# Kernel optimization log

Hardware: AMD Instinct MI355X
Metric: run time of the kernel (lower is better)

The kernel has to match this reference:

```python
import jax, jax.numpy as jnp
import numpy as np

B, IN, HID, OUT = 1024, 256, 512, 2
MU_INIT, LOGVAR_INIT = 0.0, -5.0
VAR_MIN = 1e-6


def setup_inputs() -> dict:
    key = jax.random.key(0)
    ks = jax.random.split(key, 9)
    inp = {
        "x": jax.random.normal(ks[0], (B, IN), dtype=jnp.float32),
        "w1_mu": MU_INIT + 0.1 * jax.random.normal(ks[1], (HID, IN), dtype=jnp.float32),
        "w1_logvar": LOGVAR_INIT + 0.1 * jax.random.normal(ks[2], (HID, IN), dtype=jnp.float32),
        "b1_mu": MU_INIT + 0.1 * jax.random.normal(ks[3], (HID,), dtype=jnp.float32),
        "b1_logvar": LOGVAR_INIT + 0.1 * jax.random.normal(ks[4], (HID,), dtype=jnp.float32),
        "w2_mu": MU_INIT + 0.1 * jax.random.normal(ks[5], (OUT, HID), dtype=jnp.float32),
        "w2_logvar": LOGVAR_INIT + 0.1 * jax.random.normal(ks[6], (OUT, HID), dtype=jnp.float32),
        "b2_mu": MU_INIT + 0.1 * jax.random.normal(ks[7], (OUT,), dtype=jnp.float32),
        "b2_logvar": LOGVAR_INIT + 0.1 * jax.random.normal(ks[8], (OUT,), dtype=jnp.float32),
    }
    return inp


def _bayes_linear(x, w_mu, w_logvar, b_mu, b_logvar, eps_w, eps_b):
    # Non-efficient path: per-example sampled weights (batch, out, in) and biases (batch, out)
    w_std = jnp.exp(0.5 * w_logvar)
    b_std = jnp.exp(0.5 * b_logvar)
    weights = w_mu[None, :, :] + w_std[None, :, :] * eps_w  # (B, O, I)
    biases = b_mu[None, :] + b_std[None, :] * eps_b          # (B, O)
    out = jnp.einsum("boi,bi->bo", weights, x)
    return out + biases


def reference(x, w1_mu, w1_logvar, b1_mu, b1_logvar, w2_mu, w2_logvar, b2_mu, b2_logvar):
    # Noise sampled inside forward, matching torch.randn in the module (fixed key for determinism)
    nk = jax.random.split(jax.random.key(42), 4)
    eps_w1 = jax.random.normal(nk[0], (B, HID, IN), dtype=x.dtype)
    eps_b1 = jax.random.normal(nk[1], (B, HID), dtype=x.dtype)
    eps_w2 = jax.random.normal(nk[2], (B, OUT, HID), dtype=x.dtype)
    eps_b2 = jax.random.normal(nk[3], (B, OUT), dtype=x.dtype)

    h = jax.nn.relu(_bayes_linear(x, w1_mu, w1_logvar, b1_mu, b1_logvar, eps_w1, eps_b1))
    out = _bayes_linear(h, w2_mu, w2_logvar, b2_mu, b2_logvar, eps_w2, eps_b2)  # (B, 2)
    mean = out[:, 0]
    var = jnp.maximum(jnp.exp(out[:, 1]), VAR_MIN)
    return mean, var
```

## Files before the change

kernel.cpp:

```cpp
#include <hip/hip_runtime.h>
#include <stdint.h>

#define BATCH 1024
#define IN    256
#define HID   512
#define OUT   2

#define SQRT2 1.4142135623730951

__host__ __device__ __forceinline__ uint32_t rotl32(uint32_t x, uint32_t r) {
#ifdef __HIP_DEVICE_COMPILE__
    return __builtin_rotateleft32(x, r);
#else
    return (x << r) | (x >> (32 - r));
#endif
}

__host__ __device__ __forceinline__ void threefry2x32(uint32_t k0, uint32_t k1,
                                                      uint32_t& x0, uint32_t& x1) {
    uint32_t k2 = k0 ^ k1 ^ 0x1BD11BDAu;
    x0 += k0; x1 += k1;
#define TF_R(r) { x0 += x1; x1 = rotl32(x1, (r)); x1 ^= x0; }
    TF_R(13) TF_R(15) TF_R(26) TF_R(6)   x0 += k1; x1 += k2 + 1u;
    TF_R(17) TF_R(29) TF_R(16) TF_R(24)  x0 += k2; x1 += k0 + 2u;
    TF_R(13) TF_R(15) TF_R(26) TF_R(6)   x0 += k0; x1 += k1 + 3u;
    TF_R(17) TF_R(29) TF_R(16) TF_R(24)  x0 += k1; x1 += k2 + 4u;
    TF_R(13) TF_R(15) TF_R(26) TF_R(6)   x0 += k2; x1 += k0 + 5u;
#undef TF_R
}

struct TFK {
    uint32_t k0, k1, k2, i1b, i2b, i3b, i4b, i5b;
    uint32_t k1j0, k1j1, k1j2, k1j3;
    uint32_t K01j0, K01j1, K01j2, K01j3;
    __device__ __forceinline__ TFK(uint32_t a, uint32_t b) {
        k0 = a; k1 = b; k2 = a ^ b ^ 0x1BD11BDAu;
        i1b = k2 + 1u; i2b = k0 + 2u; i3b = k1 + 3u; i4b = k2 + 4u; i5b = k0 + 5u;
        k1j0 = k1;        k1j1 = k1 + 1u;   k1j2 = k1 + 2u;   k1j3 = k1 + 3u;
        uint32_t K01 = k0 + k1;
        K01j0 = K01;      K01j1 = K01 + 1u; K01j2 = K01 + 2u; K01j3 = K01 + 3u;
    }
};

__device__ __forceinline__ uint32_t tf_core(const TFK& K, uint32_t cnt,
                                            uint32_t k1j, uint32_t K01j) {
    uint32_t t  = cnt + k1j;
    uint32_t x0 = cnt + K01j;
    uint32_t x1 = rotl32(t, 13) ^ x0;
    x0 += x1; x1 = rotl32(x1, 15) ^ x0;
    x0 += x1; x1 = rotl32(x1, 26) ^ x0;
    x0 += x1; x1 = rotl32(x1,  6) ^ x0;
    t = x1 + K.i1b; x0 = x0 + t + K.k1;  x1 = rotl32(t, 17) ^ x0;
    x0 += x1; x1 = rotl32(x1, 29) ^ x0;
    x0 += x1; x1 = rotl32(x1, 16) ^ x0;
    x0 += x1; x1 = rotl32(x1, 24) ^ x0;
    t = x1 + K.i2b; x0 = x0 + t + K.k2;  x1 = rotl32(t, 13) ^ x0;
    x0 += x1; x1 = rotl32(x1, 15) ^ x0;
    x0 += x1; x1 = rotl32(x1, 26) ^ x0;
    x0 += x1; x1 = rotl32(x1,  6) ^ x0;
    t = x1 + K.i3b; x0 = x0 + t + K.k0;  x1 = rotl32(t, 17) ^ x0;
    x0 += x1; x1 = rotl32(x1, 29) ^ x0;
    x0 += x1; x1 = rotl32(x1, 16) ^ x0;
    x0 += x1; x1 = rotl32(x1, 24) ^ x0;
    t = x1 + K.i4b; x0 = x0 + t + K.k1;  x1 = rotl32(t, 13) ^ x0;
    x0 += x1; x1 = rotl32(x1, 15) ^ x0;
    x0 += x1; x1 = rotl32(x1, 26) ^ x0;
    x0 += x1; x1 = rotl32(x1,  6) ^ x0;
    return (x0 + K.k2) ^ (x1 + K.i5b);
}
__device__ __forceinline__ uint32_t tf_bits(const TFK& K, uint32_t cnt) {
    return tf_core(K, cnt, K.k1j0, K.K01j0);
}

__device__ __forceinline__ float bits_to_normal(uint32_t bits) {
    const float LO = -0.99999994f;
#if __has_builtin(__builtin_amdgcn_alignbit)
    float m = __uint_as_float(__builtin_amdgcn_alignbit(0x7Fu, bits, 9u));
#else
    float m = __uint_as_float((bits >> 9) | 0x3f800000u);
#endif
    float u = fmaxf(LO, fmaf(m, 2.0f, -3.0f));
    float z = fmaf(-u, u, 1.0f);
    float L = __log2f(z);
    float wa = fmaf(L, -0.69314718f, -2.5f);
    float p = (float)(0.00021858087 * SQRT2);
    p = fmaf(p, wa, (float)(-0.00125372503 * SQRT2));
    p = fmaf(p, wa, (float)(-0.00417768164 * SQRT2));
    p = fmaf(p, wa, (float)(0.246640727 * SQRT2));
    p = fmaf(p, wa, (float)(1.50140941 * SQRT2));
    return p * u;
}

__global__ __launch_bounds__(256) void k_w1std(const float* __restrict__ w1_logvar,
                                               float* __restrict__ w1_std) {
    int i = blockIdx.x * 256 + threadIdx.x;
    if (i < HID * IN) w1_std[i] = __expf(0.5f * w1_logvar[i]);
}

__global__ __launch_bounds__(256, 4) void k_layer1(
    const float* __restrict__ x, const float* __restrict__ w1_mu,
    const float* __restrict__ w1_std, const float* __restrict__ b1_mu,
    const float* __restrict__ b1_logvar, float* __restrict__ h,
    uint32_t kw0, uint32_t kw1, uint32_t kb0, uint32_t kb1)
{
    __shared__ float xs[IN];
    const int b = blockIdx.y;
    const int o = blockIdx.x * 256 + threadIdx.x;
    xs[threadIdx.x] = x[b * IN + threadIdx.x];
    __syncthreads();

    const TFK Kw(kw0, kw1);
    const float4* wm4 = (const float4*)(w1_mu  + o * IN);
    const float4* ws4 = (const float4*)(w1_std + o * IN);
    const float4* x4  = (const float4*)xs;

    uint32_t c = (uint32_t)(b * HID + o) * IN;
    float acc = 0.f;

    float4 m4 = wm4[0], s4 = ws4[0], xv = x4[0];
    #pragma unroll 3
    for (int i4 = 0; i4 < IN / 4 - 1; ++i4) {
        float4 m4n = wm4[i4 + 1], s4n = ws4[i4 + 1], xvn = x4[i4 + 1];
        float e0 = bits_to_normal(tf_core(Kw, c, Kw.k1j0, Kw.K01j0));
        float e1 = bits_to_normal(tf_core(Kw, c, Kw.k1j1, Kw.K01j1));
        float e2 = bits_to_normal(tf_core(Kw, c, Kw.k1j2, Kw.K01j2));
        float e3 = bits_to_normal(tf_core(Kw, c, Kw.k1j3, Kw.K01j3));
        c += 4u;
        acc = fmaf(fmaf(s4.x, e0, m4.x), xv.x, acc);
        acc = fmaf(fmaf(s4.y, e1, m4.y), xv.y, acc);
        acc = fmaf(fmaf(s4.z, e2, m4.z), xv.z, acc);
        acc = fmaf(fmaf(s4.w, e3, m4.w), xv.w, acc);
        m4 = m4n; s4 = s4n; xv = xvn;
    }
    {
        float e0 = bits_to_normal(tf_core(Kw, c, Kw.k1j0, Kw.K01j0));
        float e1 = bits_to_normal(tf_core(Kw, c, Kw.k1j1, Kw.K01j1));
        float e2 = bits_to_normal(tf_core(Kw, c, Kw.k1j2, Kw.K01j2));
        float e3 = bits_to_normal(tf_core(Kw, c, Kw.k1j3, Kw.K01j3));
        acc = fmaf(fmaf(s4.x, e0, m4.x), xv.x, acc);
        acc = fmaf(fmaf(s4.y, e1, m4.y), xv.y, acc);
        acc = fmaf(fmaf(s4.z, e2, m4.z), xv.z, acc);
        acc = fmaf(fmaf(s4.w, e3, m4.w), xv.w, acc);
    }
    const TFK Kb(kb0, kb1);
    float eb = bits_to_normal(tf_bits(Kb, (uint32_t)(b * HID + o)));
    float hv = acc + fmaf(__expf(0.5f * b1_logvar[o]), eb, b1_mu[o]);
    h[b * HID + o] = fmaxf(hv, 0.f);
}

__global__ __launch_bounds__(256) void k_layer2(
    const float* __restrict__ h, const float* __restrict__ w2_mu,
    const float* __restrict__ w2_logvar, const float* __restrict__ b2_mu,
    const float* __restrict__ b2_logvar, float* __restrict__ out,
    uint32_t kw0, uint32_t kw1, uint32_t kb0, uint32_t kb1)
{
    const int wave = (blockIdx.x * 256 + threadIdx.x) >> 6;
    const int lane = threadIdx.x & 63;
    const int b = wave >> 1, j = wave & 1;
    const TFK Kw(kw0, kw1);

    float acc = 0.f;
    #pragma unroll
    for (int oi = 0; oi < HID / 64; ++oi) {
        int o = oi * 64 + lane;
        uint32_t c = (uint32_t)((b * OUT + j) * HID + o);
        float e = bits_to_normal(tf_bits(Kw, c));
        float m = w2_mu[j * HID + o];
        float s = __expf(0.5f * w2_logvar[j * HID + o]);
        acc = fmaf(fmaf(s, e, m), h[b * HID + o], acc);
    }
    #pragma unroll
    for (int off = 32; off > 0; off >>= 1)
        acc += __shfl_down(acc, off, 64);
    if (lane == 0) {
        const TFK Kb(kb0, kb1);
        float eb = bits_to_normal(tf_bits(Kb, (uint32_t)(b * OUT + j)));
        float o0 = acc + fmaf(__expf(0.5f * b2_logvar[j]), eb, b2_mu[j]);
        if (j == 0) out[b] = o0;
        else        out[1024 + b] = fmaxf(__expf(o0), 1e-6f);
    }
}

extern "C" void kernel_launch(void* const* d_in, const int* in_sizes, int n_in,
                              void* d_out, int out_size, void* d_ws, size_t ws_size,
                              hipStream_t stream) {
    (void)in_sizes; (void)n_in; (void)out_size; (void)ws_size;
    const float* x         = (const float*)d_in[0];
    const float* w1_mu     = (const float*)d_in[1];
    const float* w1_logvar = (const float*)d_in[2];
    const float* b1_mu     = (const float*)d_in[3];
    const float* b1_logvar = (const float*)d_in[4];
    const float* w2_mu     = (const float*)d_in[5];
    const float* w2_logvar = (const float*)d_in[6];
    const float* b2_mu     = (const float*)d_in[7];
    const float* b2_logvar = (const float*)d_in[8];
    float* out = (float*)d_out;

    float* ws_w1std = (float*)d_ws;
    float* ws_h     = (float*)d_ws + HID * IN;

    uint32_t nk[4][2];
    for (uint32_t i = 0; i < 4; ++i) {
        uint32_t a = 0u, c = i;
        threefry2x32(0u, 42u, a, c);
        nk[i][0] = a; nk[i][1] = c;
    }
    const uint32_t kw1a = nk[0][0], kw1b = nk[0][1];
    const uint32_t kb1a = nk[1][0], kb1b = nk[1][1];
    const uint32_t kw2a = nk[2][0], kw2b = nk[2][1];
    const uint32_t kb2a = nk[3][0], kb2b = nk[3][1];

    k_w1std<<<(HID * IN + 255) / 256, 256, 0, stream>>>(w1_logvar, ws_w1std);
    k_layer1<<<dim3(2, 1024), 256, 0, stream>>>(x, w1_mu, ws_w1std, b1_mu, b1_logvar,
                                                ws_h, kw1a, kw1b, kb1a, kb1b);
    k_layer2<<<512, 256, 0, stream>>>(ws_h, w2_mu, w2_logvar, b2_mu, b2_logvar,
                                      out, kw2a, kw2b, kb2a, kb2b);
}
```

Measured before the change: 316.8 us.

## Fuse layer-2 dot product into layer-1 kernel with partial sums and epilogue

Layer 1 now computes each hidden activation and immediately multiplies it by the sampled layer-2 weights. Each block reduces its two partial outputs through wave shuffles and shared memory and writes them to a small partials buffer. A tiny epilogue kernel adds the two block partials, applies the sampled output bias and writes mean and variance. This removes the hidden-activation write/read and replaces the heavier layer-2 kernel, at the cost of an extra sync and more register use in layer 1.

```diff
diff --git a/kernel.cpp b/kernel.cpp
--- a/kernel.cpp
+++ b/kernel.cpp
@@ -100,10 +100,14 @@
 __global__ __launch_bounds__(256, 4) void k_layer1(
     const float* __restrict__ x, const float* __restrict__ w1_mu,
     const float* __restrict__ w1_std, const float* __restrict__ b1_mu,
-    const float* __restrict__ b1_logvar, float* __restrict__ h,
-    uint32_t kw0, uint32_t kw1, uint32_t kb0, uint32_t kb1)
+    const float* __restrict__ b1_logvar,
+    const float* __restrict__ w2_mu, const float* __restrict__ w2_logvar,
+    float* __restrict__ partials,
+    uint32_t kw0, uint32_t kw1, uint32_t kb0, uint32_t kb1,
+    uint32_t k2w0, uint32_t k2w1)
 {
     __shared__ float xs[IN];
+    __shared__ float red[8];
     const int b = blockIdx.y;
     const int o = blockIdx.x * 256 + threadIdx.x;
     xs[threadIdx.x] = x[b * IN + threadIdx.x];
@@ -144,41 +148,44 @@
     }
     const TFK Kb(kb0, kb1);
     float eb = bits_to_normal(tf_bits(Kb, (uint32_t)(b * HID + o)));
-    float hv = acc + fmaf(__expf(0.5f * b1_logvar[o]), eb, b1_mu[o]);
-    h[b * HID + o] = fmaxf(hv, 0.f);
-}
-
-__global__ __launch_bounds__(256) void k_layer2(
-    const float* __restrict__ h, const float* __restrict__ w2_mu,
-    const float* __restrict__ w2_logvar, const float* __restrict__ b2_mu,
+    float hv = fmaxf(acc + fmaf(__expf(0.5f * b1_logvar[o]), eb, b1_mu[o]), 0.f);
+
+    const TFK K2(k2w0, k2w1);
+    uint32_t c2 = (uint32_t)(b * OUT) * HID + (uint32_t)o;
+    float e20 = bits_to_normal(tf_bits(K2, c2));
+    float e21 = bits_to_normal(tf_bits(K2, c2 + HID));
+    float a0 = fmaf(__expf(0.5f * w2_logvar[o]),       e20, w2_mu[o])       * hv;
+    float a1 = fmaf(__expf(0.5f * w2_logvar[HID + o]), e21, w2_mu[HID + o]) * hv;
+
+    #pragma unroll
+    for (int off = 32; off > 0; off >>= 1) {
+        a0 += __shfl_down(a0, off, 64);
+        a1 += __shfl_down(a1, off, 64);
+    }
+    const int wv = threadIdx.x >> 6, ln = threadIdx.x & 63;
+    if (ln == 0) { red[wv] = a0; red[4 + wv] = a1; }
+    __syncthreads();
+    if (threadIdx.x == 0) {
+        float* p = partials + ((size_t)blockIdx.x * BATCH + b) * 2;
+        p[0] = (red[0] + red[1]) + (red[2] + red[3]);
+        p[1] = (red[4] + red[5]) + (red[6] + red[7]);
+    }
+}
+
+__global__ __launch_bounds__(256) void k_epilogue(
+    const float* __restrict__ partials, const float* __restrict__ b2_mu,
     const float* __restrict__ b2_logvar, float* __restrict__ out,
-    uint32_t kw0, uint32_t kw1, uint32_t kb0, uint32_t kb1)
+    uint32_t kb0, uint32_t kb1)
 {
-    const int wave = (blockIdx.x * 256 + threadIdx.x) >> 6;
-    const int lane = threadIdx.x & 63;
-    const int b = wave >> 1, j = wave & 1;
-    const TFK Kw(kw0, kw1);
-
-    float acc = 0.f;
-    #pragma unroll
-    for (int oi = 0; oi < HID / 64; ++oi) {
-        int o = oi * 64 + lane;
-        uint32_t c = (uint32_t)((b * OUT + j) * HID + o);
-        float e = bits_to_normal(tf_bits(Kw, c));
-        float m = w2_mu[j * HID + o];
-        float s = __expf(0.5f * w2_logvar[j * HID + o]);
-        acc = fmaf(fmaf(s, e, m), h[b * HID + o], acc);
-    }
-    #pragma unroll
-    for (int off = 32; off > 0; off >>= 1)
-        acc += __shfl_down(acc, off, 64);
-    if (lane == 0) {
-        const TFK Kb(kb0, kb1);
-        float eb = bits_to_normal(tf_bits(Kb, (uint32_t)(b * OUT + j)));
-        float o0 = acc + fmaf(__expf(0.5f * b2_logvar[j]), eb, b2_mu[j]);
-        if (j == 0) out[b] = o0;
-        else        out[1024 + b] = fmaxf(__expf(o0), 1e-6f);
-    }
+    const int t = blockIdx.x * 256 + threadIdx.x;
+    const int b = t >> 1, j = t & 1;
+    float v = partials[((size_t)0 * BATCH + b) * 2 + j]
+            + partials[((size_t)1 * BATCH + b) * 2 + j];
+    const TFK Kb(kb0, kb1);
+    float eb = bits_to_normal(tf_bits(Kb, (uint32_t)(b * OUT + j)));
+    float o0 = v + fmaf(__expf(0.5f * b2_logvar[j]), eb, b2_mu[j]);
+    if (j == 0) out[b] = o0;
+    else        out[1024 + b] = fmaxf(__expf(o0), 1e-6f);
 }
 
 extern "C" void kernel_launch(void* const* d_in, const int* in_sizes, int n_in,
@@ -197,7 +204,7 @@
     float* out = (float*)d_out;
 
     float* ws_w1std = (float*)d_ws;
-    float* ws_h     = (float*)d_ws + HID * IN;
+    float* ws_part  = (float*)d_ws + HID * IN;
 
     uint32_t nk[4][2];
     for (uint32_t i = 0; i < 4; ++i) {
@@ -212,7 +219,7 @@
 
     k_w1std<<<(HID * IN + 255) / 256, 256, 0, stream>>>(w1_logvar, ws_w1std);
     k_layer1<<<dim3(2, 1024), 256, 0, stream>>>(x, w1_mu, ws_w1std, b1_mu, b1_logvar,
-                                                ws_h, kw1a, kw1b, kb1a, kb1b);
-    k_layer2<<<512, 256, 0, stream>>>(ws_h, w2_mu, w2_logvar, b2_mu, b2_logvar,
-                                      out, kw2a, kw2b, kb2a, kb2b);
-}
+                                                w2_mu, w2_logvar, ws_part,
+                                                kw1a, kw1b, kb1a, kb1b, kw2a, kw2b);
+    k_epilogue<<<8, 256, 0, stream>>>(ws_part, b2_mu, b2_logvar, out, kb2a, kb2b);
+}
```

New measurement: 316.4 us (median of 2 runs). About the same (-0.1%).
